# Optimization experiments

Hardware: AMD Instinct MI355X
Metric: run time of the kernel (lower is better)

## Reference

```python
import jax, jax.numpy as jnp
import numpy as np

# dims matching init_kwargs
B, N = 1, 2048
VOCAB, DIM, DEPTH = 32000, 1024, 4
HEADS, DIM_HEAD, WINDOW = 16, 64, 512
INNER = HEADS * DIM_HEAD          # 1024
FF_INNER = int(DIM * 4 * 2 / 3)   # 2730 (GEGLU inner)
DPB_DIM = DIM // 2
LN_EPS = 1e-5


def layernorm(x, g, b):
    m = jnp.mean(x, axis=-1, keepdims=True)
    v = jnp.mean(jnp.square(x - m), axis=-1, keepdims=True)
    return (x - m) * jax.lax.rsqrt(v + LN_EPS) * g + b


def look_around(x, backward=1, forward=0, pad_value=-1):
    # x: [b, nw, w, ...]; concat shifted windows along the window_size axis
    nw = x.shape[1]
    pads = [(0, 0), (backward, forward)] + [(0, 0)] * (x.ndim - 2)
    px = jnp.pad(x, pads, constant_values=pad_value)
    return jnp.concatenate([px[:, i:i + nw] for i in range(backward + forward + 1)], axis=2)


def dynamic_pos_bias(w1, b1, w2, b2, w3, b3, i, j):
    # MLP over scalar relative distances, then gather into [H, i, j]
    rel = jnp.arange(j, dtype=jnp.float32)[:, None]            # [j, 1]
    h = jax.nn.silu(rel @ w1 + b1)
    h = jax.nn.silu(h @ w2 + b2)
    bias = h @ w3 + b3                                          # [j, H]
    idx = jnp.abs(jnp.arange(j - i, j)[:, None] - jnp.arange(j)[None, :])  # [i, j]
    return jnp.transpose(bias[idx], (2, 0, 1))                  # [H, i, j]


def local_attention(q, k, v, attn_bias):
    # causal sliding-window attention, look_backward=1, look_forward=0, exact_windowsize=True
    # q,k,v: [B,H,N,dh]; N assumed multiple of WINDOW (autopad is a no-op then)
    b, h, n, d = q.shape
    w = WINDOW
    nw = n // w
    scale = d ** -0.5
    bq = q.reshape(b * h, nw, w, d) * scale
    bk = look_around(k.reshape(b * h, nw, w, d), pad_value=-1.0)   # [bh,nw,2w,d]
    bv = look_around(v.reshape(b * h, nw, w, d), pad_value=-1.0)
    t = jnp.arange(n).reshape(1, nw, w)
    bq_t = t[..., :, None]                                      # [1,nw,w,1]
    bq_k = look_around(t, pad_value=-1)[..., None, :]           # [1,nw,1,2w]
    # causal | exact-window | padding masks
    mask = (bq_t < bq_k) | (bq_t > bq_k + w) | (bq_k == -1)
    sim = jnp.einsum('bwid,bwjd->bwij', bq, bk)                 # [bh,nw,w,2w]
    sim = (sim.reshape(b, h, nw, w, 2 * w) + attn_bias[None, :, None]).reshape(b * h, nw, w, 2 * w)
    sim = jnp.where(mask, -jnp.finfo(sim.dtype).max, sim)
    attn = jax.nn.softmax(sim, axis=-1)
    out = jnp.einsum('bwij,bwjd->bwid', attn, bv)
    return out.reshape(b, h, n, d)


def forward(tokens, tok_emb, pos_emb, dpb_w1, dpb_b1, dpb_w2, dpb_b2, dpb_w3, dpb_b3,
            ln1_g, ln1_b, Wqkv, Wo, ln2_g, ln2_b, Wff1, Wff2, lnf_g, lnf_b, Wlogits):
    bsz, n = tokens.shape
    x = tok_emb[tokens] + pos_emb[:n]                           # [B,N,D]
    bias = dynamic_pos_bias(dpb_w1, dpb_b1, dpb_w2, dpb_b2, dpb_w3, dpb_b3, WINDOW, 2 * WINDOW)

    def split_heads(t):
        return t.reshape(bsz, n, HEADS, DIM_HEAD).transpose(0, 2, 1, 3)

    for l in range(DEPTH):
        # LocalMHA (prenorm) + residual
        h = layernorm(x, ln1_g[l], ln1_b[l])
        q, k, v = jnp.split(h @ Wqkv[l], 3, axis=-1)
        o = local_attention(split_heads(q), split_heads(k), split_heads(v), bias)
        o = o.transpose(0, 2, 1, 3).reshape(bsz, n, INNER)
        x = x + o @ Wo[l]
        # GEGLU FFN (prenorm inside FeedForward) + residual
        h = layernorm(x, ln2_g[l], ln2_b[l])
        a, gate = jnp.split(h @ Wff1[l], 2, axis=-1)
        x = x + (a * jax.nn.gelu(gate, approximate=False)) @ Wff2[l]

    return layernorm(x, lnf_g, lnf_b) @ Wlogits                 # [B,N,V]


def setup_inputs() -> dict:
    key = jax.random.key(0)
    ks = iter(jax.random.split(key, 16))
    s = 0.02
    rn = lambda *shape: jax.random.normal(next(ks), shape, dtype=jnp.float32) * s
    return {
        'tokens': jax.random.randint(next(ks), (B, N), 0, VOCAB, dtype=jnp.int32),
        'tok_emb': rn(VOCAB, DIM),
        'pos_emb': rn(N, DIM),
        'dpb_w1': rn(1, DPB_DIM), 'dpb_b1': jnp.zeros((DPB_DIM,), jnp.float32),
        'dpb_w2': rn(DPB_DIM, DPB_DIM), 'dpb_b2': jnp.zeros((DPB_DIM,), jnp.float32),
        'dpb_w3': rn(DPB_DIM, HEADS), 'dpb_b3': jnp.zeros((HEADS,), jnp.float32),
        'ln1_g': jnp.ones((DEPTH, DIM), jnp.float32), 'ln1_b': jnp.zeros((DEPTH, DIM), jnp.float32),
        'Wqkv': rn(DEPTH, DIM, 3 * INNER),
        'Wo': rn(DEPTH, INNER, DIM),
        'ln2_g': jnp.ones((DEPTH, DIM), jnp.float32), 'ln2_b': jnp.zeros((DEPTH, DIM), jnp.float32),
        'Wff1': rn(DEPTH, DIM, 2 * FF_INNER),
        'Wff2': rn(DEPTH, FF_INNER, DIM),
        'lnf_g': jnp.ones((DIM,), jnp.float32), 'lnf_b': jnp.zeros((DIM,), jnp.float32),
        'Wlogits': rn(DIM, VOCAB),
    }


def reference(tokens, tok_emb, pos_emb, dpb_w1, dpb_b1, dpb_w2, dpb_b2, dpb_w3, dpb_b3,
              ln1_g, ln1_b, Wqkv, Wo, ln2_g, ln2_b, Wff1, Wff2, lnf_g, lnf_b, Wlogits):
    return forward(tokens, tok_emb, pos_emb, dpb_w1, dpb_b1, dpb_w2, dpb_b2, dpb_w3, dpb_b3,
                   ln1_g, ln1_b, Wqkv, Wo, ln2_g, ln2_b, Wff1, Wff2, lnf_g, lnf_b, Wlogits)
```

## Files before the change

### kernel.cpp

```cpp
#include <hip/hip_runtime.h>
#include <cstdint>

#define DEV __device__ __forceinline__

typedef __attribute__((ext_vector_type(8))) short bf16x8;
typedef __attribute__((ext_vector_type(4))) short bf16x4;
typedef __attribute__((ext_vector_type(4))) float f32x4;

DEV float bf2f(unsigned short u) { return __uint_as_float(((unsigned)u) << 16); }
DEV unsigned short f2bf(float f) {
  unsigned u = __float_as_uint(f);
  u += 0x7FFFu + ((u >> 16) & 1u);
  return (unsigned short)(u >> 16);
}

DEV void gload_lds16(const void* g, void* lds) {
  __builtin_amdgcn_global_load_lds(
      (const __attribute__((address_space(1))) unsigned int*)g,
      (__attribute__((address_space(3))) unsigned int*)lds, 16, 0, 0);
}

__global__ __launch_bounds__(256) void k_embed(const int* __restrict__ tokens,
    const float* __restrict__ tok_emb, const float* __restrict__ pos_emb,
    float* __restrict__ x) {
  int n = blockIdx.x;
  int tok = tokens[n];
  int c = threadIdx.x * 4;
  float4 a = *(const float4*)(tok_emb + (long)tok * 1024 + c);
  float4 p = *(const float4*)(pos_emb + (long)n * 1024 + c);
  float4 r;
  r.x = a.x + p.x; r.y = a.y + p.y; r.z = a.z + p.z; r.w = a.w + p.w;
  *(float4*)(x + (long)n * 1024 + c) = r;
}

__global__ __launch_bounds__(256) void k_ln(const float* __restrict__ x,
    const float* __restrict__ g, const float* __restrict__ b,
    unsigned short* __restrict__ out) {
  __shared__ float red[8];
  int row = blockIdx.x, t = threadIdx.x;
  const float* xr = x + (long)row * 1024;
  float4 v = *(const float4*)(xr + t * 4);
  float s = v.x + v.y + v.z + v.w;
#pragma unroll
  for (int off = 32; off; off >>= 1) s += __shfl_xor(s, off);
  if ((t & 63) == 0) red[t >> 6] = s;
  __syncthreads();
  float mean = (red[0] + red[1] + red[2] + red[3]) * (1.0f / 1024.0f);
  float dx = v.x - mean, dy = v.y - mean, dz = v.z - mean, dw = v.w - mean;
  float sq = dx * dx + dy * dy + dz * dz + dw * dw;
#pragma unroll
  for (int off = 32; off; off >>= 1) sq += __shfl_xor(sq, off);
  if ((t & 63) == 0) red[4 + (t >> 6)] = sq;
  __syncthreads();
  float var = (red[4] + red[5] + red[6] + red[7]) * (1.0f / 1024.0f);
  float inv = rsqrtf(var + 1e-5f);
  int c = t * 4;
  float4 gv = *(const float4*)(g + c);
  float4 bv = *(const float4*)(b + c);
  ushort4 o;
  o.x = f2bf(dx * inv * gv.x + bv.x);
  o.y = f2bf(dy * inv * gv.y + bv.y);
  o.z = f2bf(dz * inv * gv.z + bv.z);
  o.w = f2bf(dw * inv * gv.w + bv.w);
  *(ushort4*)(out + (long)row * 1024 + c) = o;
}

__global__ __launch_bounds__(256) void k_wconv(const float* __restrict__ src,
    unsigned short* __restrict__ dst, int K, int N, int Kp, int Np,
    long sstride, long dstride) {
  __shared__ float tile[32][33];
  const float* s = src + (long)blockIdx.z * sstride;
  unsigned short* d = dst + (long)blockIdx.z * dstride;
  int n0 = blockIdx.x * 32, k0 = blockIdx.y * 32;
  int t = threadIdx.x;
  int r = t >> 3, c4 = (t & 7) * 4;
  int k = k0 + r, n = n0 + c4;
  float4 v = make_float4(0.f, 0.f, 0.f, 0.f);
  if (k < K && n < N) v = *(const float4*)(s + (long)k * N + n);
  tile[r][c4 + 0] = v.x;
  tile[r][c4 + 1] = v.y;
  tile[r][c4 + 2] = v.z;
  tile[r][c4 + 3] = v.w;
  __syncthreads();
  int nrow = n0 + r;
  ushort4 o;
  o.x = f2bf(tile[c4 + 0][r]);
  o.y = f2bf(tile[c4 + 1][r]);
  o.z = f2bf(tile[c4 + 2][r]);
  o.w = f2bf(tile[c4 + 3][r]);
  (void)Np;
  *(ushort4*)(d + (long)nrow * Kp + k0 + c4) = o;
}

__global__ __launch_bounds__(256) void k_dpb(const float* __restrict__ w1,
    const float* __restrict__ b1, const float* __restrict__ w2,
    const float* __restrict__ b2, const float* __restrict__ w3,
    const float* __restrict__ b3, float* __restrict__ table) {
  __shared__ float h1[512], h2[512];
  int r = blockIdx.x, t = threadIdx.x;
  float rf = (float)r;
  for (int c = t; c < 512; c += 256) {
    float v = rf * w1[c] + b1[c];
    h1[c] = v / (1.0f + __expf(-v));
  }
  __syncthreads();
  for (int c = t; c < 512; c += 256) {
    float acc = b2[c];
    for (int k2 = 0; k2 < 512; ++k2) acc = fmaf(h1[k2], w2[(long)k2 * 512 + c], acc);
    h2[c] = acc / (1.0f + __expf(-acc));
  }
  __syncthreads();
  if (t < 16) {
    float acc = b3[t];
    for (int k2 = 0; k2 < 512; ++k2) acc = fmaf(h2[k2], w3[k2 * 16 + t], acc);
    table[r * 16 + t] = acc;
  }
}

__global__ __launch_bounds__(256) void k_glu(const unsigned short* __restrict__ ff,
    unsigned short* __restrict__ u) {
  int row = blockIdx.x, t = threadIdx.x;
  const unsigned short* fr = ff + (long)row * 5504;
  unsigned short* ur = u + (long)row * 2752;
  for (int c = t * 4; c < 2752; c += 1024) {
    ushort4 av = *(const ushort4*)(fr + c);
    ushort2 g0 = *(const ushort2*)(fr + 2730 + c);
    ushort2 g1 = *(const ushort2*)(fr + 2730 + c + 2);
    float aa[4] = {bf2f(av.x), bf2f(av.y), bf2f(av.z), bf2f(av.w)};
    float gg[4] = {bf2f(g0.x), bf2f(g0.y), bf2f(g1.x), bf2f(g1.y)};
    ushort4 o;
    unsigned short* op = (unsigned short*)&o;
#pragma unroll
    for (int e = 0; e < 4; ++e) {
      float val = 0.0f;
      if (c + e < 2730)
        val = aa[e] * (0.5f * gg[e] * (1.0f + erff(gg[e] * 0.70710678118654752f)));
      op[e] = f2bf(val);
    }
    *(ushort4*)(ur + c) = o;
  }
}

__global__ __launch_bounds__(256, 2) void k_attn_mfma(
    const unsigned short* __restrict__ qkv, const float* __restrict__ table,
    unsigned short* __restrict__ o) {
  __shared__ unsigned short Ks[64 * 64];
  __shared__ unsigned short Vt[64 * 72];
  __shared__ unsigned short Ps[4][16 * 72];
  __shared__ float biasl[1024];
  const int qt = blockIdx.x, h = blockIdx.y, wi = blockIdx.z;
  const int iw0 = qt * 64;
  const int t = threadIdx.x;
  const int w = t >> 6, l = t & 63;
  const int lq = l & 15, lk = l >> 4;

  for (int i = t; i < 1024; i += 256) biasl[i] = table[i * 16 + h];

  const unsigned short* qp = qkv + (long)(wi * 512 + iw0 + w * 16 + lq) * 3072 + h * 64;
  bf16x8 qf0 = *(const bf16x8*)(qp + lk * 8);
  bf16x8 qf1 = *(const bf16x8*)(qp + 32 + lk * 8);

  f32x4 oacc[4] = {};
  float mrun[4] = {-3.0e38f, -3.0e38f, -3.0e38f, -3.0e38f};
  float srun[4] = {};

  const int kt0 = (wi == 0) ? 8 : qt;
  const int kt1 = qt + 8;
  for (int kt = kt0; kt <= kt1; ++kt) {
    const int ktbase = kt * 64;
    const long kgbase = (long)((wi - 1) * 512 + ktbase);
    __syncthreads();
    {
      const unsigned short* Kg = qkv + kgbase * 3072 + 1024 + h * 64;
#pragma unroll
      for (int s2 = 0; s2 < 2; ++s2) {
        int g = s2 * 4 + w;
        int row = g * 8 + (l >> 3);
        int gch = (l & 7) ^ (row & 7);
        gload_lds16(Kg + (long)row * 3072 + gch * 8, &Ks[g * 512]);
      }
    }
    {
      int kp = t & 31, dg = t >> 5;
      const unsigned short* Vg =
          qkv + (kgbase + 2 * kp) * 3072 + 2048 + h * 64 + dg * 8;
      bf16x8 a0 = *(const bf16x8*)Vg;
      bf16x8 a1 = *(const bf16x8*)(Vg + 3072);
#pragma unroll
      for (int e = 0; e < 8; ++e) {
        unsigned pack = ((unsigned)(unsigned short)a0[e]) |
                        (((unsigned)(unsigned short)a1[e]) << 16);
        *(unsigned*)&Vt[(dg * 8 + e) * 72 + 2 * kp] = pack;
      }
    }
    asm volatile("s_waitcnt vmcnt(0)" ::: "memory");
    __syncthreads();

    f32x4 sacc[4] = {};
#pragma unroll
    for (int ct = 0; ct < 4; ++ct) {
      int krow = ct * 16 + lq;
      bf16x8 kf0 = *(const bf16x8*)&Ks[krow * 64 + (((0 + lk) ^ (krow & 7)) * 8)];
      bf16x8 kf1 = *(const bf16x8*)&Ks[krow * 64 + (((4 + lk) ^ (krow & 7)) * 8)];
      sacc[ct] = __builtin_amdgcn_mfma_f32_16x16x32_bf16(qf0, kf0, sacc[ct], 0, 0, 0);
      sacc[ct] = __builtin_amdgcn_mfma_f32_16x16x32_bf16(qf1, kf1, sacc[ct], 0, 0, 0);
    }

#pragma unroll
    for (int r = 0; r < 4; ++r) {
      const int iw = iw0 + w * 16 + lk * 4 + r;
      float sc[4];
#pragma unroll
      for (int ct = 0; ct < 4; ++ct) {
        int jj = ktbase + ct * 16 + lq;
        int di = 512 + iw - jj;
        int dic = min(max(di, 0), 1023);
        bool allowed = (jj >= iw) && (jj <= iw + 512);
        float v = sacc[ct][r] * 0.125f + biasl[dic];
        sc[ct] = allowed ? v : -3.0e38f;
      }
      float mx = fmaxf(fmaxf(sc[0], sc[1]), fmaxf(sc[2], sc[3]));
      mx = fmaxf(mx, __shfl_xor(mx, 1));
      mx = fmaxf(mx, __shfl_xor(mx, 2));
      mx = fmaxf(mx, __shfl_xor(mx, 4));
      mx = fmaxf(mx, __shfl_xor(mx, 8));
      float mnew = fmaxf(mrun[r], mx);
      float f = __expf(mrun[r] - mnew);
      mrun[r] = mnew;
      float rs = 0.0f;
#pragma unroll
      for (int ct = 0; ct < 4; ++ct) {
        float pv = __expf(sc[ct] - mnew);
        rs += pv;
        Ps[w][(lk * 4 + r) * 72 + ct * 16 + lq] = f2bf(pv);
      }
      rs += __shfl_xor(rs, 1);
      rs += __shfl_xor(rs, 2);
      rs += __shfl_xor(rs, 4);
      rs += __shfl_xor(rs, 8);
      srun[r] = srun[r] * f + rs;
#pragma unroll
      for (int dt = 0; dt < 4; ++dt) oacc[dt][r] *= f;
    }
    asm volatile("s_waitcnt lgkmcnt(0)" ::: "memory");

#pragma unroll
    for (int ks = 0; ks < 2; ++ks) {
      bf16x4 pa0 = *(const bf16x4*)&Ps[w][lq * 72 + ks * 32 + lk * 8];
      bf16x4 pa1 = *(const bf16x4*)&Ps[w][lq * 72 + ks * 32 + lk * 8 + 4];
      bf16x8 pa = __builtin_shufflevector(pa0, pa1, 0, 1, 2, 3, 4, 5, 6, 7);
#pragma unroll
      for (int dt = 0; dt < 4; ++dt) {
        int drow = dt * 16 + lq;
        bf16x4 vb0 = *(const bf16x4*)&Vt[drow * 72 + ks * 32 + lk * 8];
        bf16x4 vb1 = *(const bf16x4*)&Vt[drow * 72 + ks * 32 + lk * 8 + 4];
        bf16x8 vb = __builtin_shufflevector(vb0, vb1, 0, 1, 2, 3, 4, 5, 6, 7);
        oacc[dt] = __builtin_amdgcn_mfma_f32_16x16x32_bf16(pa, vb, oacc[dt], 0, 0, 0);
      }
    }
  }

  unsigned short* ob =
      o + (long)(wi * 512 + iw0 + w * 16 + lk * 4) * 1024 + h * 64 + lq;
#pragma unroll
  for (int r = 0; r < 4; ++r) {
    float inv = 1.0f / srun[r];
#pragma unroll
    for (int dt = 0; dt < 4; ++dt)
      ob[(long)r * 1024 + dt * 16] = f2bf(oacc[dt][r] * inv);
  }
}

template <int EPI>
__global__ __launch_bounds__(256, 2) void k_gemm(const unsigned short* __restrict__ A,
    const unsigned short* __restrict__ BT, void* __restrict__ Cout,
    int N, int K, int nbm) {
  __shared__ unsigned short As[128 * 64];
  __shared__ unsigned short Bs[128 * 64];
  const int nwg = gridDim.x;
  const int orig = blockIdx.x;
  const int q8 = nwg >> 3, r8 = nwg & 7;
  const int xcd = orig & 7, i8 = orig >> 3;
  const int wgid = (xcd < r8 ? xcd * (q8 + 1) : r8 * (q8 + 1) + (xcd - r8) * q8) + i8;
  const int bm = wgid % nbm;
  const int bn = wgid / nbm;
  const int t = threadIdx.x;
  const int w = t >> 6, l = t & 63;
  const int wm = w >> 1, wn = w & 1;
  const int lrow = l >> 3, lch = l & 7;
  const int lq = l & 15, lk = l >> 4;
  f32x4 acc[4][4] = {};
  const long arow0 = (long)bm * 128, brow0 = (long)bn * 128;
  for (int kt = 0; kt < K; kt += 64) {
    __syncthreads();
#pragma unroll
    for (int s2 = 0; s2 < 4; ++s2) {
      int grp = s2 * 4 + w;
      int r = grp * 8 + lrow;
      int gch = lch ^ lrow;
      gload_lds16(A + (arow0 + r) * K + kt + gch * 8, &As[grp * 512]);
      gload_lds16(BT + (brow0 + r) * K + kt + gch * 8, &Bs[grp * 512]);
    }
    asm volatile("s_waitcnt vmcnt(0)" ::: "memory");
    __syncthreads();
#pragma unroll
    for (int kk = 0; kk < 2; ++kk) {
      bf16x8 af[4], bfr[4];
#pragma unroll
      for (int i = 0; i < 4; ++i) {
        int ra = wm * 64 + i * 16 + lq;
        af[i] = *(const bf16x8*)&As[ra * 64 + (((kk * 4 + lk) ^ (ra & 7)) * 8)];
        int rb = wn * 64 + i * 16 + lq;
        bfr[i] = *(const bf16x8*)&Bs[rb * 64 + (((kk * 4 + lk) ^ (rb & 7)) * 8)];
      }
#pragma unroll
      for (int i = 0; i < 4; ++i)
#pragma unroll
        for (int j = 0; j < 4; ++j)
          acc[i][j] = __builtin_amdgcn_mfma_f32_16x16x32_bf16(af[i], bfr[j],
                                                              acc[i][j], 0, 0, 0);
    }
  }
  const int rbase = bm * 128 + wm * 64 + lk * 4;
  const int cbase = bn * 128 + wn * 64 + lq;
#pragma unroll
  for (int i = 0; i < 4; ++i) {
#pragma unroll
    for (int j = 0; j < 4; ++j) {
#pragma unroll
      for (int r2 = 0; r2 < 4; ++r2) {
        long row = rbase + i * 16 + r2;
        long col = cbase + j * 16;
        float v = acc[i][j][r2];
        if (EPI == 0)
          ((unsigned short*)Cout)[row * N + col] = f2bf(v);
        else if (EPI == 1)
          ((float*)Cout)[row * N + col] += v;
        else
          ((float*)Cout)[row * N + col] = v;
      }
    }
  }
}

extern "C" void kernel_launch(void* const* d_in, const int* in_sizes, int n_in,
                              void* d_out, int out_size, void* d_ws, size_t ws_size,
                              hipStream_t stream) {
  (void)in_sizes; (void)n_in; (void)out_size; (void)ws_size;
  const int* tokens   = (const int*)d_in[0];
  const float* tok_emb = (const float*)d_in[1];
  const float* pos_emb = (const float*)d_in[2];
  const float* dpb_w1 = (const float*)d_in[3];
  const float* dpb_b1 = (const float*)d_in[4];
  const float* dpb_w2 = (const float*)d_in[5];
  const float* dpb_b2 = (const float*)d_in[6];
  const float* dpb_w3 = (const float*)d_in[7];
  const float* dpb_b3 = (const float*)d_in[8];
  const float* ln1_g  = (const float*)d_in[9];
  const float* ln1_b  = (const float*)d_in[10];
  const float* Wqkv   = (const float*)d_in[11];
  const float* Wo     = (const float*)d_in[12];
  const float* ln2_g  = (const float*)d_in[13];
  const float* ln2_b  = (const float*)d_in[14];
  const float* Wff1   = (const float*)d_in[15];
  const float* Wff2   = (const float*)d_in[16];
  const float* lnf_g  = (const float*)d_in[17];
  const float* lnf_b  = (const float*)d_in[18];
  const float* Wlog   = (const float*)d_in[19];
  float* out = (float*)d_out;

  char* p = (char*)d_ws;
  auto carve = [&](size_t bytes) {
    char* q = p;
    p += (bytes + 255) & ~(size_t)255;
    return (void*)q;
  };
  unsigned short* WqkvT = (unsigned short*)carve((size_t)4 * 3072 * 1024 * 2);
  unsigned short* WoT   = (unsigned short*)carve((size_t)4 * 1024 * 1024 * 2);
  unsigned short* Wff1T = (unsigned short*)carve((size_t)4 * 5504 * 1024 * 2);
  unsigned short* Wff2T = (unsigned short*)carve((size_t)4 * 1024 * 2752 * 2);
  unsigned short* WlogT = (unsigned short*)carve((size_t)32000 * 1024 * 2);
  float*          x     = (float*)carve((size_t)2048 * 1024 * 4);
  unsigned short* hbuf  = (unsigned short*)carve((size_t)2048 * 1024 * 2);
  unsigned short* qkv   = (unsigned short*)carve((size_t)2048 * 3072 * 2);
  unsigned short* ao    = (unsigned short*)carve((size_t)2048 * 1024 * 2);
  unsigned short* ff    = (unsigned short*)carve((size_t)2048 * 5504 * 2);
  unsigned short* ubuf  = (unsigned short*)carve((size_t)2048 * 2752 * 2);
  float*          table = (float*)carve((size_t)1024 * 16 * 4);

  k_wconv<<<dim3(3072 / 32, 1024 / 32, 4), 256, 0, stream>>>(
      Wqkv, WqkvT, 1024, 3072, 1024, 3072, (long)1024 * 3072, (long)3072 * 1024);
  k_wconv<<<dim3(1024 / 32, 1024 / 32, 4), 256, 0, stream>>>(
      Wo, WoT, 1024, 1024, 1024, 1024, (long)1024 * 1024, (long)1024 * 1024);
  k_wconv<<<dim3(5504 / 32, 1024 / 32, 4), 256, 0, stream>>>(
      Wff1, Wff1T, 1024, 5460, 1024, 5504, (long)1024 * 5460, (long)5504 * 1024);
  k_wconv<<<dim3(1024 / 32, 2752 / 32, 4), 256, 0, stream>>>(
      Wff2, Wff2T, 2730, 1024, 2752, 1024, (long)2730 * 1024, (long)1024 * 2752);
  k_wconv<<<dim3(32000 / 32, 1024 / 32, 1), 256, 0, stream>>>(
      Wlog, WlogT, 1024, 32000, 1024, 32000, 0L, 0L);

  k_dpb<<<1024, 256, 0, stream>>>(dpb_w1, dpb_b1, dpb_w2, dpb_b2, dpb_w3, dpb_b3, table);
  k_embed<<<2048, 256, 0, stream>>>(tokens, tok_emb, pos_emb, x);

  const int NBM = 16;
  for (int l = 0; l < 4; ++l) {
    k_ln<<<2048, 256, 0, stream>>>(x, ln1_g + l * 1024, ln1_b + l * 1024, hbuf);
    k_gemm<0><<<dim3(NBM * (3072 / 128)), 256, 0, stream>>>(
        hbuf, WqkvT + (long)l * 3072 * 1024, qkv, 3072, 1024, NBM);
    k_attn_mfma<<<dim3(8, 16, 4), 256, 0, stream>>>(qkv, table, ao);
    k_gemm<1><<<dim3(NBM * (1024 / 128)), 256, 0, stream>>>(
        ao, WoT + (long)l * 1024 * 1024, x, 1024, 1024, NBM);
    k_ln<<<2048, 256, 0, stream>>>(x, ln2_g + l * 1024, ln2_b + l * 1024, hbuf);
    k_gemm<0><<<dim3(NBM * (5504 / 128)), 256, 0, stream>>>(
        hbuf, Wff1T + (long)l * 5504 * 1024, ff, 5504, 1024, NBM);
    k_glu<<<2048, 256, 0, stream>>>(ff, ubuf);
    k_gemm<1><<<dim3(NBM * (1024 / 128)), 256, 0, stream>>>(
        ubuf, Wff2T + (long)l * 1024 * 2752, x, 1024, 2752, NBM);
  }
  k_ln<<<2048, 256, 0, stream>>>(x, lnf_g, lnf_b, hbuf);
  k_gemm<2><<<dim3(NBM * (32000 / 128)), 256, 0, stream>>>(
      hbuf, WlogT, out, 32000, 1024, NBM);
}
```

Baseline: 1.183 ms.

## Fuse GEGLU into FF1 GEMM epilogue, merge prep kernels, row-per-wave layernorm

Wff1 columns are interleaved during weight conversion so that each value column sits next to its gate column. The FF1 GEMM epilogue can then compute GELU-gating with a lane shuffle and write the halved output directly, which removes the separate GLU kernel and the 2048x5504 intermediate buffer. All weight conversions, the position-bias MLP and the embedding are merged into one launch. LayerNorm now handles four rows per block, one row per wavefront, with no shared-memory reduction. Half the lanes in the fused epilogue stay idle, and the GEMM writes become strided 2-byte stores.

```diff
diff --git a/kernel.cpp b/kernel.cpp
--- a/kernel.cpp
+++ b/kernel.cpp
@@ -20,124 +20,136 @@
       (__attribute__((address_space(3))) unsigned int*)lds, 16, 0, 0);
 }
 
-__global__ __launch_bounds__(256) void k_embed(const int* __restrict__ tokens,
-    const float* __restrict__ tok_emb, const float* __restrict__ pos_emb,
-    float* __restrict__ x) {
-  int n = blockIdx.x;
-  int tok = tokens[n];
-  int c = threadIdx.x * 4;
-  float4 a = *(const float4*)(tok_emb + (long)tok * 1024 + c);
-  float4 p = *(const float4*)(pos_emb + (long)n * 1024 + c);
-  float4 r;
-  r.x = a.x + p.x; r.y = a.y + p.y; r.z = a.z + p.z; r.w = a.w + p.w;
-  *(float4*)(x + (long)n * 1024 + c) = r;
-}
-
-__global__ __launch_bounds__(256) void k_ln(const float* __restrict__ x,
-    const float* __restrict__ g, const float* __restrict__ b,
-    unsigned short* __restrict__ out) {
-  __shared__ float red[8];
-  int row = blockIdx.x, t = threadIdx.x;
-  const float* xr = x + (long)row * 1024;
-  float4 v = *(const float4*)(xr + t * 4);
-  float s = v.x + v.y + v.z + v.w;
-#pragma unroll
-  for (int off = 32; off; off >>= 1) s += __shfl_xor(s, off);
-  if ((t & 63) == 0) red[t >> 6] = s;
-  __syncthreads();
-  float mean = (red[0] + red[1] + red[2] + red[3]) * (1.0f / 1024.0f);
-  float dx = v.x - mean, dy = v.y - mean, dz = v.z - mean, dw = v.w - mean;
-  float sq = dx * dx + dy * dy + dz * dz + dw * dw;
-#pragma unroll
-  for (int off = 32; off; off >>= 1) sq += __shfl_xor(sq, off);
-  if ((t & 63) == 0) red[4 + (t >> 6)] = sq;
-  __syncthreads();
-  float var = (red[4] + red[5] + red[6] + red[7]) * (1.0f / 1024.0f);
-  float inv = rsqrtf(var + 1e-5f);
-  int c = t * 4;
-  float4 gv = *(const float4*)(g + c);
-  float4 bv = *(const float4*)(b + c);
-  ushort4 o;
-  o.x = f2bf(dx * inv * gv.x + bv.x);
-  o.y = f2bf(dy * inv * gv.y + bv.y);
-  o.z = f2bf(dz * inv * gv.z + bv.z);
-  o.w = f2bf(dw * inv * gv.w + bv.w);
-  *(ushort4*)(out + (long)row * 1024 + c) = o;
-}
-
-__global__ __launch_bounds__(256) void k_wconv(const float* __restrict__ src,
-    unsigned short* __restrict__ dst, int K, int N, int Kp, int Np,
-    long sstride, long dstride) {
-  __shared__ float tile[32][33];
-  const float* s = src + (long)blockIdx.z * sstride;
-  unsigned short* d = dst + (long)blockIdx.z * dstride;
-  int n0 = blockIdx.x * 32, k0 = blockIdx.y * 32;
-  int t = threadIdx.x;
+__global__ __launch_bounds__(256) void k_prep(
+    const int* __restrict__ tokens, const float* __restrict__ tok_emb,
+    const float* __restrict__ pos_emb, float* __restrict__ x,
+    const float* __restrict__ w1, const float* __restrict__ b1,
+    const float* __restrict__ w2, const float* __restrict__ b2,
+    const float* __restrict__ w3, const float* __restrict__ b3,
+    float* __restrict__ table,
+    const float* __restrict__ Wqkv, unsigned short* __restrict__ WqkvT,
+    const float* __restrict__ Wo, unsigned short* __restrict__ WoT,
+    const float* __restrict__ Wff1, unsigned short* __restrict__ Wff1T,
+    const float* __restrict__ Wff2, unsigned short* __restrict__ Wff2T,
+    const float* __restrict__ Wlog, unsigned short* __restrict__ WlogT) {
+  __shared__ float smem[1056];
+  int b = blockIdx.x, t = threadIdx.x;
+  if (b < 2048) {
+    int tok = tokens[b];
+    int c = t * 4;
+    float4 a = *(const float4*)(tok_emb + (long)tok * 1024 + c);
+    float4 p = *(const float4*)(pos_emb + (long)b * 1024 + c);
+    float4 r;
+    r.x = a.x + p.x; r.y = a.y + p.y; r.z = a.z + p.z; r.w = a.w + p.w;
+    *(float4*)(x + (long)b * 1024 + c) = r;
+    return;
+  }
+  b -= 2048;
+  if (b < 1024) {
+    float* h1 = smem;
+    float* h2 = smem + 512;
+    float rf = (float)b;
+    for (int c = t; c < 512; c += 256) {
+      float v = rf * w1[c] + b1[c];
+      h1[c] = v / (1.0f + __expf(-v));
+    }
+    __syncthreads();
+    for (int c = t; c < 512; c += 256) {
+      float acc = b2[c];
+      for (int k2 = 0; k2 < 512; ++k2) acc = fmaf(h1[k2], w2[(long)k2 * 512 + c], acc);
+      h2[c] = acc / (1.0f + __expf(-acc));
+    }
+    __syncthreads();
+    if (t < 16) {
+      float acc = b3[t];
+      for (int k2 = 0; k2 < 512; ++k2) acc = fmaf(h2[k2], w3[k2 * 16 + t], acc);
+      table[b * 16 + t] = acc;
+    }
+    return;
+  }
+  b -= 1024;
+  const float* src; unsigned short* dst;
+  int K, N, Kp, nx, ny, mode;
+  long ss, ds;
+  if (b < 12288) {
+    src = Wqkv; dst = WqkvT; K = 1024; N = 3072; Kp = 1024;
+    nx = 96; ny = 32; mode = 0; ss = 1024L * 3072; ds = 3072L * 1024;
+  } else if ((b -= 12288) < 4096) {
+    src = Wo; dst = WoT; K = 1024; N = 1024; Kp = 1024;
+    nx = 32; ny = 32; mode = 0; ss = 1024L * 1024; ds = 1024L * 1024;
+  } else if ((b -= 4096) < 22016) {
+    src = Wff1; dst = Wff1T; K = 1024; N = 5460; Kp = 1024;
+    nx = 172; ny = 32; mode = 1; ss = 1024L * 5460; ds = 5504L * 1024;
+  } else if ((b -= 22016) < 11008) {
+    src = Wff2; dst = Wff2T; K = 2730; N = 1024; Kp = 2752;
+    nx = 32; ny = 86; mode = 0; ss = 2730L * 1024; ds = 1024L * 2752;
+  } else {
+    b -= 11008;
+    src = Wlog; dst = WlogT; K = 1024; N = 32000; Kp = 1024;
+    nx = 1000; ny = 32; mode = 0; ss = 0; ds = 0;
+  }
+  int z = b / (nx * ny);
+  int rem = b % (nx * ny);
+  int n0 = (rem % nx) * 32, k0 = (rem / nx) * 32;
+  src += (long)z * ss;
+  dst += (long)z * ds;
+  float (*tile)[33] = (float(*)[33])smem;
   int r = t >> 3, c4 = (t & 7) * 4;
   int k = k0 + r, n = n0 + c4;
   float4 v = make_float4(0.f, 0.f, 0.f, 0.f);
-  if (k < K && n < N) v = *(const float4*)(s + (long)k * N + n);
+  if (k < K && n < N) v = *(const float4*)(src + (long)k * N + n);
   tile[r][c4 + 0] = v.x;
   tile[r][c4 + 1] = v.y;
   tile[r][c4 + 2] = v.z;
   tile[r][c4 + 3] = v.w;
   __syncthreads();
   int nrow = n0 + r;
+  if (mode) nrow = nrow < 2730 ? 2 * nrow : (nrow < 5460 ? 2 * (nrow - 2730) + 1 : nrow);
   ushort4 o;
   o.x = f2bf(tile[c4 + 0][r]);
   o.y = f2bf(tile[c4 + 1][r]);
   o.z = f2bf(tile[c4 + 2][r]);
   o.w = f2bf(tile[c4 + 3][r]);
-  (void)Np;
-  *(ushort4*)(d + (long)nrow * Kp + k0 + c4) = o;
-}
-
-__global__ __launch_bounds__(256) void k_dpb(const float* __restrict__ w1,
-    const float* __restrict__ b1, const float* __restrict__ w2,
-    const float* __restrict__ b2, const float* __restrict__ w3,
-    const float* __restrict__ b3, float* __restrict__ table) {
-  __shared__ float h1[512], h2[512];
-  int r = blockIdx.x, t = threadIdx.x;
-  float rf = (float)r;
-  for (int c = t; c < 512; c += 256) {
-    float v = rf * w1[c] + b1[c];
-    h1[c] = v / (1.0f + __expf(-v));
-  }
-  __syncthreads();
-  for (int c = t; c < 512; c += 256) {
-    float acc = b2[c];
-    for (int k2 = 0; k2 < 512; ++k2) acc = fmaf(h1[k2], w2[(long)k2 * 512 + c], acc);
-    h2[c] = acc / (1.0f + __expf(-acc));
-  }
-  __syncthreads();
-  if (t < 16) {
-    float acc = b3[t];
-    for (int k2 = 0; k2 < 512; ++k2) acc = fmaf(h2[k2], w3[k2 * 16 + t], acc);
-    table[r * 16 + t] = acc;
-  }
-}
-
-__global__ __launch_bounds__(256) void k_glu(const unsigned short* __restrict__ ff,
-    unsigned short* __restrict__ u) {
-  int row = blockIdx.x, t = threadIdx.x;
-  const unsigned short* fr = ff + (long)row * 5504;
-  unsigned short* ur = u + (long)row * 2752;
-  for (int c = t * 4; c < 2752; c += 1024) {
-    ushort4 av = *(const ushort4*)(fr + c);
-    ushort2 g0 = *(const ushort2*)(fr + 2730 + c);
-    ushort2 g1 = *(const ushort2*)(fr + 2730 + c + 2);
-    float aa[4] = {bf2f(av.x), bf2f(av.y), bf2f(av.z), bf2f(av.w)};
-    float gg[4] = {bf2f(g0.x), bf2f(g0.y), bf2f(g1.x), bf2f(g1.y)};
+  *(ushort4*)(dst + (long)nrow * Kp + k0 + c4) = o;
+}
+
+__global__ __launch_bounds__(256) void k_ln4(const float* __restrict__ x,
+    const float* __restrict__ g, const float* __restrict__ b,
+    unsigned short* __restrict__ out) {
+  const int row = blockIdx.x * 4 + (threadIdx.x >> 6);
+  const int l = threadIdx.x & 63;
+  const float* xr = x + (long)row * 1024 + l * 16;
+  float4 v[4];
+#pragma unroll
+  for (int e = 0; e < 4; ++e) v[e] = ((const float4*)xr)[e];
+  float s = 0.0f;
+#pragma unroll
+  for (int e = 0; e < 4; ++e) s += v[e].x + v[e].y + v[e].z + v[e].w;
+#pragma unroll
+  for (int off = 32; off; off >>= 1) s += __shfl_xor(s, off);
+  float mean = s * (1.0f / 1024.0f);
+  float sq = 0.0f;
+#pragma unroll
+  for (int e = 0; e < 4; ++e) {
+    float a0 = v[e].x - mean, a1 = v[e].y - mean, a2 = v[e].z - mean, a3 = v[e].w - mean;
+    sq += a0 * a0 + a1 * a1 + a2 * a2 + a3 * a3;
+  }
+#pragma unroll
+  for (int off = 32; off; off >>= 1) sq += __shfl_xor(sq, off);
+  float inv = rsqrtf(sq * (1.0f / 1024.0f) + 1e-5f);
+  const float* gr = g + l * 16;
+  const float* br = b + l * 16;
+  unsigned short* orow = out + (long)row * 1024 + l * 16;
+#pragma unroll
+  for (int e = 0; e < 4; ++e) {
+    float4 gv = ((const float4*)gr)[e];
+    float4 bv = ((const float4*)br)[e];
     ushort4 o;
-    unsigned short* op = (unsigned short*)&o;
-#pragma unroll
-    for (int e = 0; e < 4; ++e) {
-      float val = 0.0f;
-      if (c + e < 2730)
-        val = aa[e] * (0.5f * gg[e] * (1.0f + erff(gg[e] * 0.70710678118654752f)));
-      op[e] = f2bf(val);
-    }
-    *(ushort4*)(ur + c) = o;
+    o.x = f2bf((v[e].x - mean) * inv * gv.x + bv.x);
+    o.y = f2bf((v[e].y - mean) * inv * gv.y + bv.y);
+    o.z = f2bf((v[e].z - mean) * inv * gv.z + bv.z);
+    o.w = f2bf((v[e].w - mean) * inv * gv.w + bv.w);
+    ((ushort4*)orow)[e] = o;
   }
 }
 
@@ -332,12 +344,20 @@
         long row = rbase + i * 16 + r2;
         long col = cbase + j * 16;
         float v = acc[i][j][r2];
-        if (EPI == 0)
+        if (EPI == 0) {
           ((unsigned short*)Cout)[row * N + col] = f2bf(v);
-        else if (EPI == 1)
+        } else if (EPI == 1) {
           ((float*)Cout)[row * N + col] += v;
-        else
+        } else if (EPI == 2) {
           ((float*)Cout)[row * N + col] = v;
+        } else {
+          float gpart = __shfl_xor(v, 1);
+          if ((lq & 1) == 0) {
+            float uval =
+                v * (0.5f * gpart * (1.0f + erff(gpart * 0.70710678118654752f)));
+            ((unsigned short*)Cout)[row * (N >> 1) + (col >> 1)] = f2bf(uval);
+          }
+        }
       }
     }
   }
@@ -384,40 +404,28 @@
   unsigned short* hbuf  = (unsigned short*)carve((size_t)2048 * 1024 * 2);
   unsigned short* qkv   = (unsigned short*)carve((size_t)2048 * 3072 * 2);
   unsigned short* ao    = (unsigned short*)carve((size_t)2048 * 1024 * 2);
-  unsigned short* ff    = (unsigned short*)carve((size_t)2048 * 5504 * 2);
   unsigned short* ubuf  = (unsigned short*)carve((size_t)2048 * 2752 * 2);
   float*          table = (float*)carve((size_t)1024 * 16 * 4);
 
-  k_wconv<<<dim3(3072 / 32, 1024 / 32, 4), 256, 0, stream>>>(
-      Wqkv, WqkvT, 1024, 3072, 1024, 3072, (long)1024 * 3072, (long)3072 * 1024);
-  k_wconv<<<dim3(1024 / 32, 1024 / 32, 4), 256, 0, stream>>>(
-      Wo, WoT, 1024, 1024, 1024, 1024, (long)1024 * 1024, (long)1024 * 1024);
-  k_wconv<<<dim3(5504 / 32, 1024 / 32, 4), 256, 0, stream>>>(
-      Wff1, Wff1T, 1024, 5460, 1024, 5504, (long)1024 * 5460, (long)5504 * 1024);
-  k_wconv<<<dim3(1024 / 32, 2752 / 32, 4), 256, 0, stream>>>(
-      Wff2, Wff2T, 2730, 1024, 2752, 1024, (long)2730 * 1024, (long)1024 * 2752);
-  k_wconv<<<dim3(32000 / 32, 1024 / 32, 1), 256, 0, stream>>>(
-      Wlog, WlogT, 1024, 32000, 1024, 32000, 0L, 0L);
-
-  k_dpb<<<1024, 256, 0, stream>>>(dpb_w1, dpb_b1, dpb_w2, dpb_b2, dpb_w3, dpb_b3, table);
-  k_embed<<<2048, 256, 0, stream>>>(tokens, tok_emb, pos_emb, x);
+  k_prep<<<84480, 256, 0, stream>>>(
+      tokens, tok_emb, pos_emb, x, dpb_w1, dpb_b1, dpb_w2, dpb_b2, dpb_w3,
+      dpb_b3, table, Wqkv, WqkvT, Wo, WoT, Wff1, Wff1T, Wff2, Wff2T, Wlog, WlogT);
 
   const int NBM = 16;
   for (int l = 0; l < 4; ++l) {
-    k_ln<<<2048, 256, 0, stream>>>(x, ln1_g + l * 1024, ln1_b + l * 1024, hbuf);
+    k_ln4<<<512, 256, 0, stream>>>(x, ln1_g + l * 1024, ln1_b + l * 1024, hbuf);
     k_gemm<0><<<dim3(NBM * (3072 / 128)), 256, 0, stream>>>(
         hbuf, WqkvT + (long)l * 3072 * 1024, qkv, 3072, 1024, NBM);
     k_attn_mfma<<<dim3(8, 16, 4), 256, 0, stream>>>(qkv, table, ao);
     k_gemm<1><<<dim3(NBM * (1024 / 128)), 256, 0, stream>>>(
         ao, WoT + (long)l * 1024 * 1024, x, 1024, 1024, NBM);
-    k_ln<<<2048, 256, 0, stream>>>(x, ln2_g + l * 1024, ln2_b + l * 1024, hbuf);
-    k_gemm<0><<<dim3(NBM * (5504 / 128)), 256, 0, stream>>>(
-        hbuf, Wff1T + (long)l * 5504 * 1024, ff, 5504, 1024, NBM);
-    k_glu<<<2048, 256, 0, stream>>>(ff, ubuf);
+    k_ln4<<<512, 256, 0, stream>>>(x, ln2_g + l * 1024, ln2_b + l * 1024, hbuf);
+    k_gemm<3><<<dim3(NBM * (5504 / 128)), 256, 0, stream>>>(
+        hbuf, Wff1T + (long)l * 5504 * 1024, ubuf, 5504, 1024, NBM);
     k_gemm<1><<<dim3(NBM * (1024 / 128)), 256, 0, stream>>>(
         ubuf, Wff2T + (long)l * 1024 * 2752, x, 1024, 2752, NBM);
   }
-  k_ln<<<2048, 256, 0, stream>>>(x, lnf_g, lnf_b, hbuf);
+  k_ln4<<<512, 256, 0, stream>>>(x, lnf_g, lnf_b, hbuf);
   k_gemm<2><<<dim3(NBM * (32000 / 128)), 256, 0, stream>>>(
       hbuf, WlogT, out, 32000, 1024, NBM);
 }
```

Measured after the change: 1.148 ms. 2.9% less time.
